# Kernel tuning notes

Hardware: AMD Instinct MI355X
Metric: run time of the kernel (lower is better)

Reference implementation:

```python
import jax, jax.numpy as jnp
import numpy as np

N = 100000   # nodes
E = 1600000  # edges
IN = 128     # input feature dim
HID = 64     # hidden = IN // 2
OUT = 8      # output_size
B = 16384    # lookup batch


def sage_conv(x, src, dst, W_l, W_r, b, n):
    # PyG SAGEConv (aggr='mean', root_weight=True):
    # out = lin_l(mean_{j in N(i)} x_j) + lin_r(x_i)
    msgs = x[src]                                              # [E, F] gather
    agg = jax.ops.segment_sum(msgs, dst, num_segments=n)       # [N, F] scatter-add
    deg = jax.ops.segment_sum(jnp.ones((src.shape[0],), x.dtype), dst, num_segments=n)
    mean = agg / jnp.maximum(deg, 1.0)[:, None]                # zero-degree -> 0
    return mean @ W_l + x @ W_r + b


def setup_inputs() -> dict:
    key = jax.random.key(0)
    ks = jax.random.split(key, 10)
    node_feats = jax.random.normal(ks[0], (N, IN), dtype=jnp.float32)
    edge_index = jax.random.randint(ks[1], (2, E), 0, N, dtype=jnp.int64)
    idx = jax.random.randint(ks[2], (B,), 0, N, dtype=jnp.int64)
    dropout_mask = jax.random.uniform(ks[3], (N, HID), dtype=jnp.float32)
    s1 = 1.0 / np.sqrt(IN)
    s2 = 1.0 / np.sqrt(HID)
    W1_l = jax.random.normal(ks[4], (IN, HID), dtype=jnp.float32) * s1
    W1_r = jax.random.normal(ks[5], (IN, HID), dtype=jnp.float32) * s1
    b1 = jnp.zeros((HID,), dtype=jnp.float32)
    W2_l = jax.random.normal(ks[6], (HID, OUT), dtype=jnp.float32) * s2
    W2_r = jax.random.normal(ks[7], (HID, OUT), dtype=jnp.float32) * s2
    b2 = jnp.zeros((OUT,), dtype=jnp.float32)
    return {"node_feats": node_feats, "edge_index": edge_index, "idx": idx,
            "dropout_mask": dropout_mask, "W1_l": W1_l, "W1_r": W1_r, "b1": b1,
            "W2_l": W2_l, "W2_r": W2_r, "b2": b2}


def reference(node_feats, edge_index, idx, dropout_mask, W1_l, W1_r, b1, W2_l, W2_r, b2):
    n = node_feats.shape[0]
    src, dst = edge_index[0], edge_index[1]
    h = sage_conv(node_feats, src, dst, W1_l, W1_r, b1, n)     # [N, HID]
    h = jax.nn.relu(h)
    keep = (dropout_mask > 0.5).astype(h.dtype)                # F.dropout p=0.5
    h = h * keep * 2.0                                         # inverted dropout scale 1/(1-p)
    emb = sage_conv(h, src, dst, W2_l, W2_r, b2, n)            # [N, OUT]
    return emb[idx]                                            # [B, OUT]
```

## Files before the change

kernel.cpp:

```cpp
#include <hip/hip_runtime.h>
#include <hip/hip_fp16.h>

#define IN_F 128
#define HID_F 64
#define OUT_F 8

#define BSHIFT 7
#define BGRAN 128
#define BCAP 2688
#define NBUK_MAX 784
#define CHUNK 4096
#define EPT (CHUNK / 256)
#define CEPT ((BCAP + 255) / 256)

#if defined(__has_builtin)
#if __has_builtin(__builtin_amdgcn_fdot2)
#define HAS_FDOT2 1
#endif
#endif

typedef _Float16 h2v __attribute__((ext_vector_type(2)));

__global__ __launch_bounds__(1024) void init_bcur(int* __restrict__ bcur, int nbuk) {
  int t = threadIdx.x;
  if (t < nbuk) bcur[t] = t * BCAP;
}

__global__ __launch_bounds__(256) void bucket_scatter(
    const int* __restrict__ src, const int* __restrict__ dst,
    int* __restrict__ bcur, int* __restrict__ ebuf, int n_edges) {
  __shared__ int hist[NBUK_MAX];
  __shared__ int base[NBUK_MAX];
  int t = threadIdx.x;
  for (int i = t; i < NBUK_MAX; i += 256) hist[i] = 0;
  __syncthreads();
  int e0 = blockIdx.x * CHUNK;
  int pk[EPT];
  int bk[EPT];
#pragma unroll
  for (int k = 0; k < EPT; ++k) {
    int e = e0 + k * 256 + t;
    if (e < n_edges) {
      int s = src[e];
      int d = dst[e];
      bk[k] = d >> BSHIFT;
      pk[k] = ((d & (BGRAN - 1)) << 24) | s;
      atomicAdd(&hist[bk[k]], 1);
    } else {
      bk[k] = -1;
    }
  }
  __syncthreads();
  for (int i = t; i < NBUK_MAX; i += 256) {
    int c = hist[i];
    base[i] = c ? atomicAdd(&bcur[i], c) : 0;
  }
  __syncthreads();
  for (int i = t; i < NBUK_MAX; i += 256) hist[i] = 0;
  __syncthreads();
#pragma unroll
  for (int k = 0; k < EPT; ++k) {
    if (bk[k] >= 0) {
      int r = atomicAdd(&hist[bk[k]], 1);
      ebuf[base[bk[k]] + r] = pk[k];
    }
  }
}

__global__ __launch_bounds__(256) void bucket_csr(
    const int* __restrict__ ebuf, const int* __restrict__ bcur,
    int* __restrict__ offs_f, int* __restrict__ deg_i,
    int* __restrict__ csr_src, int n_nodes) {
  __shared__ int hist[BGRAN];
  __shared__ int cur[BGRAN];
  __shared__ int s[BGRAN];
  __shared__ int lds_src[BCAP];
  int b = blockIdx.x;
  int t = threadIdx.x;
  if (t < BGRAN) hist[t] = 0;
  __syncthreads();
  int beg = b * BCAP;
  int cnt = bcur[b] - beg;
  int pk[CEPT];
  int np = 0;
  for (int j = t; j < cnt; j += 256) {
    pk[np] = ebuf[beg + j];
    atomicAdd(&hist[(unsigned)pk[np] >> 24], 1);
    ++np;
  }
  __syncthreads();
  if (t < BGRAN) s[t] = hist[t];
  __syncthreads();
  for (int d = 1; d < BGRAN; d <<= 1) {
    int v = 0;
    if (t >= d && t < BGRAN) v = s[t - d];
    __syncthreads();
    if (t >= d && t < BGRAN) s[t] += v;
    __syncthreads();
  }
  if (t < BGRAN) {
    int excl = (t == 0) ? 0 : s[t - 1];
    cur[t] = excl;
    int node = b * BGRAN + t;
    if (node < n_nodes) {
      offs_f[node] = beg + excl;
      deg_i[node] = hist[t];
    }
  }
  __syncthreads();
  for (int i = 0; i < np; ++i) {
    int dl = (unsigned)pk[i] >> 24;
    int p = atomicAdd(&cur[dl], 1);
    lds_src[p] = pk[i] & 0xFFFFFF;
  }
  __syncthreads();
  for (int j = t; j < cnt; j += 256) csr_src[beg + j] = lds_src[j];
}

#define BM 128
#define BK 32
__global__ __launch_bounds__(256, 4) void k1_proj(
    const float* __restrict__ x,
    const float* __restrict__ Wl,
    const float* __restrict__ Wr,
    const float* __restrict__ b1,
    const float* __restrict__ mask,
    __half* __restrict__ y1h,
    __half* __restrict__ r1h,
    unsigned long long* __restrict__ mbits,
    int n_nodes) {
  __shared__ h2v XS2[BK / 2][BM];
  __shared__ h2v WS2[BK / 2][128];
  int tid = threadIdx.x;
  int tx = tid & 15;
  int ty = tid >> 4;
  int n0 = blockIdx.x * BM;

  {
    int w = tid >> 6;
    int lane = tid & 63;
    for (int i = w; i < BM; i += 4) {
      int node = n0 + i;
      if (node < n_nodes) {
        float mv = mask[(size_t)node * HID_F + lane];
        unsigned long long bits = __ballot(mv > 0.5f);
        if (lane == 0) mbits[node] = bits;
      }
    }
  }

  float acc[8][8];
#pragma unroll
  for (int i = 0; i < 8; ++i)
#pragma unroll
    for (int j = 0; j < 8; ++j) acc[i][j] = 0.f;

  for (int kb = 0; kb < IN_F; kb += BK) {
    {
      int nn0 = tid >> 3;
      int k4 = (tid & 7) * 4;
      int kp0 = (tid & 7) * 2;
#pragma unroll
      for (int p = 0; p < 4; ++p) {
        int nn = nn0 + p * 32;
        int gs = min(n0 + nn, n_nodes - 1);
        float4 v = *(const float4*)(x + (size_t)gs * IN_F + kb + k4);
        XS2[kp0][nn] = h2v{(_Float16)v.x, (_Float16)v.y};
        XS2[kp0 + 1][nn] = h2v{(_Float16)v.z, (_Float16)v.w};
      }
    }
    {
#pragma unroll
      for (int p = 0; p < 2; ++p) {
        int sidx = tid + p * 256;
        int kp = sidx >> 5;
        int col = (sidx & 31) * 4;
        int k0 = kb + kp * 2;
        const float* pa = (col < 64) ? (Wl + (size_t)k0 * HID_F + col)
                                     : (Wr + (size_t)k0 * HID_F + (col - 64));
        const float* pb = (col < 64) ? (Wl + (size_t)(k0 + 1) * HID_F + col)
                                     : (Wr + (size_t)(k0 + 1) * HID_F + (col - 64));
        float4 wa = *(const float4*)pa;
        float4 wb = *(const float4*)pb;
        WS2[kp][col + 0] = h2v{(_Float16)wa.x, (_Float16)wb.x};
        WS2[kp][col + 1] = h2v{(_Float16)wa.y, (_Float16)wb.y};
        WS2[kp][col + 2] = h2v{(_Float16)wa.z, (_Float16)wb.z};
        WS2[kp][col + 3] = h2v{(_Float16)wa.w, (_Float16)wb.w};
      }
    }
    __syncthreads();
#pragma unroll 4
    for (int kp = 0; kp < BK / 2; ++kp) {
      h2v xv[8], wv[8];
#pragma unroll
      for (int i = 0; i < 8; ++i) xv[i] = XS2[kp][ty * 8 + i];
#pragma unroll
      for (int j = 0; j < 8; ++j) wv[j] = WS2[kp][tx * 8 + j];
#pragma unroll
      for (int i = 0; i < 8; ++i)
#pragma unroll
        for (int j = 0; j < 8; ++j) {
#ifdef HAS_FDOT2
          acc[i][j] = __builtin_amdgcn_fdot2(xv[i], wv[j], acc[i][j], false);
#else
          acc[i][j] += (float)xv[i][0] * (float)wv[j][0] +
                       (float)xv[i][1] * (float)wv[j][1];
#endif
        }
    }
    __syncthreads();
  }

  int outb = tx * 8;
  bool isR = (outb >= HID_F);
  int ob = isR ? outb - HID_F : outb;
  __half* dbuf = isR ? r1h : y1h;
  float bb[8];
#pragma unroll
  for (int j = 0; j < 8; ++j) bb[j] = isR ? b1[ob + j] : 0.f;
#pragma unroll
  for (int i = 0; i < 8; ++i) {
    int node = n0 + ty * 8 + i;
    if (node < n_nodes) {
      __half hh[8];
#pragma unroll
      for (int j = 0; j < 8; ++j) hh[j] = __float2half(acc[i][j] + bb[j]);
      *(uint4*)(dbuf + (size_t)node * HID_F + ob) = *(uint4*)hh;
    }
  }
}

__global__ __launch_bounds__(256) void agg1_fused(
    const __half* __restrict__ y1h,
    const __half* __restrict__ r1h,
    const int* __restrict__ deg_i,
    const int* __restrict__ offs,
    const int* __restrict__ csr_src,
    const unsigned long long* __restrict__ mbits,
    __half* __restrict__ h_h,
    int n_nodes) {
  int node = (blockIdx.x * blockDim.x + threadIdx.x) >> 6;
  int lane = threadIdx.x & 63;
  if (node >= n_nodes) return;
  int q = lane >> 4;
  int f4 = lane & 15;
  int beg = offs[node];
  int d = deg_i[node];
  const int* cp = csr_src + beg;
  float a0 = 0.f, a1 = 0.f, a2 = 0.f, a3 = 0.f;
  int j = 0;
  for (; j + 16 <= d; j += 16) {
    int s0 = cp[j + q];
    int s1 = cp[j + 4 + q];
    int s2 = cp[j + 8 + q];
    int s3 = cp[j + 12 + q];
    uint2 g0 = *(const uint2*)(y1h + (size_t)s0 * HID_F + f4 * 4);
    uint2 g1 = *(const uint2*)(y1h + (size_t)s1 * HID_F + f4 * 4);
    uint2 g2 = *(const uint2*)(y1h + (size_t)s2 * HID_F + f4 * 4);
    uint2 g3 = *(const uint2*)(y1h + (size_t)s3 * HID_F + f4 * 4);
    float2 p0 = __half22float2(*(const __half2*)&g0.x);
    float2 p1 = __half22float2(*(const __half2*)&g0.y);
    float2 p2 = __half22float2(*(const __half2*)&g1.x);
    float2 p3 = __half22float2(*(const __half2*)&g1.y);
    float2 p4 = __half22float2(*(const __half2*)&g2.x);
    float2 p5 = __half22float2(*(const __half2*)&g2.y);
    float2 p6 = __half22float2(*(const __half2*)&g3.x);
    float2 p7 = __half22float2(*(const __half2*)&g3.y);
    a0 += (p0.x + p2.x) + (p4.x + p6.x);
    a1 += (p0.y + p2.y) + (p4.y + p6.y);
    a2 += (p1.x + p3.x) + (p5.x + p7.x);
    a3 += (p1.y + p3.y) + (p5.y + p7.y);
  }
  for (; j < d; j += 4) {
    int e = j + q;
    if (e < d) {
      int s = cp[e];
      uint2 g = *(const uint2*)(y1h + (size_t)s * HID_F + f4 * 4);
      float2 p0 = __half22float2(*(const __half2*)&g.x);
      float2 p1 = __half22float2(*(const __half2*)&g.y);
      a0 += p0.x; a1 += p0.y; a2 += p1.x; a3 += p1.y;
    }
  }
  a0 += __shfl_xor(a0, 16); a0 += __shfl_xor(a0, 32);
  a1 += __shfl_xor(a1, 16); a1 += __shfl_xor(a1, 32);
  a2 += __shfl_xor(a2, 16); a2 += __shfl_xor(a2, 32);
  a3 += __shfl_xor(a3, 16); a3 += __shfl_xor(a3, 32);
  if (q == 0) {
    float inv = 1.0f / fmaxf((float)d, 1.0f);
    size_t o = (size_t)node * HID_F + f4 * 4;
    uint2 rg = *(const uint2*)(r1h + o);
    float2 r01 = __half22float2(*(const __half2*)&rg.x);
    float2 r23 = __half22float2(*(const __half2*)&rg.y);
    unsigned long long mb = mbits[node];
    float vx = fmaxf(a0 * inv + r01.x, 0.f);
    float vy = fmaxf(a1 * inv + r01.y, 0.f);
    float vz = fmaxf(a2 * inv + r23.x, 0.f);
    float vw = fmaxf(a3 * inv + r23.y, 0.f);
    int fb = f4 * 4;
    vx = ((mb >> (fb + 0)) & 1ull) ? vx * 2.f : 0.f;
    vy = ((mb >> (fb + 1)) & 1ull) ? vy * 2.f : 0.f;
    vz = ((mb >> (fb + 2)) & 1ull) ? vz * 2.f : 0.f;
    vw = ((mb >> (fb + 3)) & 1ull) ? vw * 2.f : 0.f;
    __half hh[4] = {__float2half(vx), __float2half(vy),
                    __float2half(vz), __float2half(vw)};
    *(uint2*)(h_h + o) = *(uint2*)hh;
  }
}

__global__ __launch_bounds__(256) void k3b_z(
    const __half* __restrict__ h_h,
    const float* __restrict__ W2l,
    __half* __restrict__ z,
    int n_nodes) {
  __shared__ float WS[HID_F][OUT_F];
  int tid = threadIdx.x;
  if (tid < 128) {
    float4 w = *(const float4*)(W2l + tid * 4);
    *(float4*)&WS[tid >> 1][(tid & 1) * 4] = w;
  }
  __syncthreads();
  int node = blockIdx.x * blockDim.x + tid;
  if (node >= n_nodes) return;
  const __half* hr = h_h + (size_t)node * HID_F;
  float acc[8] = {0, 0, 0, 0, 0, 0, 0, 0};
  for (int k = 0; k < HID_F; k += 8) {
    uint4 hv = *(const uint4*)(hr + k);
    float2 f0 = __half22float2(*(const __half2*)&hv.x);
    float2 f1 = __half22float2(*(const __half2*)&hv.y);
    float2 f2 = __half22float2(*(const __half2*)&hv.z);
    float2 f3 = __half22float2(*(const __half2*)&hv.w);
    float hh[8] = {f0.x, f0.y, f1.x, f1.y, f2.x, f2.y, f3.x, f3.y};
#pragma unroll
    for (int j = 0; j < 8; ++j) {
      float4 w0 = *(const float4*)&WS[k + j][0];
      float4 w1 = *(const float4*)&WS[k + j][4];
      acc[0] += hh[j] * w0.x; acc[1] += hh[j] * w0.y;
      acc[2] += hh[j] * w0.z; acc[3] += hh[j] * w0.w;
      acc[4] += hh[j] * w1.x; acc[5] += hh[j] * w1.y;
      acc[6] += hh[j] * w1.z; acc[7] += hh[j] * w1.w;
    }
  }
  __half hz[8];
#pragma unroll
  for (int j = 0; j < 8; ++j) hz[j] = __float2half(acc[j]);
  *(uint4*)(z + (size_t)node * OUT_F) = *(uint4*)hz;
}

__global__ __launch_bounds__(256) void out_fused(
    const int* __restrict__ idx,
    const __half* __restrict__ z,
    const int* __restrict__ deg_i,
    const int* __restrict__ offs,
    const int* __restrict__ csr_src,
    const __half* __restrict__ h_h,
    const float* __restrict__ W2r,
    const float* __restrict__ b2,
    float* __restrict__ out,
    int n_batch) {
  int b = (blockIdx.x * blockDim.x + threadIdx.x) >> 6;
  int lane = threadIdx.x & 63;
  if (b >= n_batch) return;
  int i = idx[b];
  int e8 = lane >> 3;
  int o = lane & 7;
  int beg = offs[i];
  int d = deg_i[i];
  float acc = 0.f;
  for (int j = e8; j < d; j += 8) {
    int s = csr_src[beg + j];
    acc += __half2float(z[(size_t)s * OUT_F + o]);
  }
  float dv = fmaxf((float)d, 1.0f);
  float v = acc / dv;
  uint4 hv = *(const uint4*)(h_h + (size_t)i * HID_F + e8 * 8);
  float2 f0 = __half22float2(*(const __half2*)&hv.x);
  float2 f1 = __half22float2(*(const __half2*)&hv.y);
  float2 f2 = __half22float2(*(const __half2*)&hv.z);
  float2 f3 = __half22float2(*(const __half2*)&hv.w);
  float hh[8] = {f0.x, f0.y, f1.x, f1.y, f2.x, f2.y, f3.x, f3.y};
#pragma unroll
  for (int jj = 0; jj < 8; ++jj) {
    int k = e8 * 8 + jj;
    v += hh[jj] * W2r[k * OUT_F + o];
  }
  v += __shfl_xor(v, 8);
  v += __shfl_xor(v, 16);
  v += __shfl_xor(v, 32);
  if (e8 == 0) out[(size_t)b * OUT_F + o] = v + b2[o];
}

extern "C" void kernel_launch(void* const* d_in, const int* in_sizes, int n_in,
                              void* d_out, int out_size, void* d_ws, size_t ws_size,
                              hipStream_t stream) {
  const float* x    = (const float*)d_in[0];
  const int*   ei   = (const int*)d_in[1];
  const int*   idx  = (const int*)d_in[2];
  const float* mask = (const float*)d_in[3];
  const float* W1l  = (const float*)d_in[4];
  const float* W1r  = (const float*)d_in[5];
  const float* b1   = (const float*)d_in[6];
  const float* W2l  = (const float*)d_in[7];
  const float* W2r  = (const float*)d_in[8];
  const float* b2   = (const float*)d_in[9];
  float* out = (float*)d_out;

  int n_nodes = in_sizes[0] / IN_F;
  int n_edges = in_sizes[1] / 2;
  int n_batch = in_sizes[2];
  const int* src = ei;
  const int* dst = ei + n_edges;

  int nbuk = (n_nodes + BGRAN - 1) / BGRAN;
  int nchunk = (n_edges + CHUNK - 1) / CHUNK;

  char* ws = (char*)d_ws;
  size_t off = 0;
  __half* y1h = (__half*)(ws + off); off += (size_t)n_nodes * HID_F * 2;
  __half* r1h = (__half*)(ws + off); off += (size_t)n_nodes * HID_F * 2;
  __half* h_h = (__half*)(ws + off); off += (size_t)n_nodes * HID_F * 2;
  __half* z   = (__half*)(ws + off); off += (size_t)n_nodes * OUT_F * 2;
  unsigned long long* mbits = (unsigned long long*)(ws + off); off += (size_t)n_nodes * 8;
  int* ebuf    = (int*)(ws + off); off += (size_t)nbuk * BCAP * 4;
  int* csr_src = (int*)(ws + off); off += (size_t)nbuk * BCAP * 4;
  int* deg_i   = (int*)(ws + off); off += (size_t)n_nodes * 4;
  int* offs_f  = (int*)(ws + off); off += (size_t)n_nodes * 4;
  int* bcur    = (int*)(ws + off); off += NBUK_MAX * 4;

  init_bcur<<<1, 1024, 0, stream>>>(bcur, nbuk);
  bucket_scatter<<<nchunk, 256, 0, stream>>>(src, dst, bcur, ebuf, n_edges);
  k1_proj<<<(n_nodes + BM - 1) / BM, 256, 0, stream>>>(
      x, W1l, W1r, b1, mask, y1h, r1h, mbits, n_nodes);
  bucket_csr<<<nbuk, 256, 0, stream>>>(ebuf, bcur, offs_f, deg_i, csr_src, n_nodes);

  {
    long long th = (long long)n_nodes * HID_F;
    agg1_fused<<<(int)((th + 255) / 256), 256, 0, stream>>>(
        y1h, r1h, deg_i, offs_f, csr_src, mbits, h_h, n_nodes);
  }

  k3b_z<<<(n_nodes + 255) / 256, 256, 0, stream>>>(h_h, W2l, z, n_nodes);
  {
    long long th = (long long)n_batch * 64;
    out_fused<<<(int)((th + 255) / 256), 256, 0, stream>>>(
        idx, z, deg_i, offs_f, csr_src, h_h, W2r, b2, out, n_batch);
  }
}
```

Measured before the change: 267.2 us.

## Use MFMA 16x16x32 f16 for layer-1 projection with pre-transposed fp16 weights

Replaces the fdot2-based register-tiled GEMM in k1_proj with MFMA 16x16x32 f16 instructions. Each wave computes 16 rows against all 128 output columns. A new w_prep kernel transposes and converts W1_l/W1_r to fp16 once per call, and B fragments are read directly from global memory. The x tile is staged in padded LDS in a single pass. This should cut ALU time for the projection, but output stores become scalar half writes and it adds a small serial prep kernel.

```diff
diff --git a/kernel.cpp b/kernel.cpp
--- a/kernel.cpp
+++ b/kernel.cpp
@@ -13,13 +13,8 @@
 #define EPT (CHUNK / 256)
 #define CEPT ((BCAP + 255) / 256)
 
-#if defined(__has_builtin)
-#if __has_builtin(__builtin_amdgcn_fdot2)
-#define HAS_FDOT2 1
-#endif
-#endif
-
-typedef _Float16 h2v __attribute__((ext_vector_type(2)));
+typedef _Float16 f16x8 __attribute__((ext_vector_type(8)));
+typedef float f32x4 __attribute__((ext_vector_type(4)));
 
 __global__ __launch_bounds__(1024) void init_bcur(int* __restrict__ bcur, int nbuk) {
   int t = threadIdx.x;
@@ -117,115 +112,86 @@
   for (int j = t; j < cnt; j += 256) csr_src[beg + j] = lds_src[j];
 }
 
-#define BM 128
-#define BK 32
-__global__ __launch_bounds__(256, 4) void k1_proj(
+__global__ __launch_bounds__(128) void w_prep(
+    const float* __restrict__ Wl, const float* __restrict__ Wr,
+    _Float16* __restrict__ Wt) {
+  int n = threadIdx.x;
+  for (int k = 0; k < IN_F; ++k) {
+    float v = (n < HID_F) ? Wl[k * HID_F + n] : Wr[k * HID_F + (n - HID_F)];
+    Wt[n * IN_F + k] = (_Float16)v;
+  }
+}
+
+#define K1_ROWS 64
+#define XSTRIDE 136
+__global__ __launch_bounds__(256) void k1_proj(
     const float* __restrict__ x,
-    const float* __restrict__ Wl,
-    const float* __restrict__ Wr,
+    const _Float16* __restrict__ Wt,
     const float* __restrict__ b1,
     const float* __restrict__ mask,
     __half* __restrict__ y1h,
     __half* __restrict__ r1h,
     unsigned long long* __restrict__ mbits,
     int n_nodes) {
-  __shared__ h2v XS2[BK / 2][BM];
-  __shared__ h2v WS2[BK / 2][128];
+  __shared__ _Float16 XS[K1_ROWS * XSTRIDE];
   int tid = threadIdx.x;
-  int tx = tid & 15;
-  int ty = tid >> 4;
-  int n0 = blockIdx.x * BM;
-
-  {
-    int w = tid >> 6;
-    int lane = tid & 63;
-    for (int i = w; i < BM; i += 4) {
-      int node = n0 + i;
-      if (node < n_nodes) {
-        float mv = mask[(size_t)node * HID_F + lane];
-        unsigned long long bits = __ballot(mv > 0.5f);
-        if (lane == 0) mbits[node] = bits;
-      }
-    }
-  }
-
-  float acc[8][8];
-#pragma unroll
-  for (int i = 0; i < 8; ++i)
-#pragma unroll
-    for (int j = 0; j < 8; ++j) acc[i][j] = 0.f;
-
-  for (int kb = 0; kb < IN_F; kb += BK) {
-    {
-      int nn0 = tid >> 3;
-      int k4 = (tid & 7) * 4;
-      int kp0 = (tid & 7) * 2;
-#pragma unroll
-      for (int p = 0; p < 4; ++p) {
-        int nn = nn0 + p * 32;
-        int gs = min(n0 + nn, n_nodes - 1);
-        float4 v = *(const float4*)(x + (size_t)gs * IN_F + kb + k4);
-        XS2[kp0][nn] = h2v{(_Float16)v.x, (_Float16)v.y};
-        XS2[kp0 + 1][nn] = h2v{(_Float16)v.z, (_Float16)v.w};
-      }
-    }
-    {
-#pragma unroll
-      for (int p = 0; p < 2; ++p) {
-        int sidx = tid + p * 256;
-        int kp = sidx >> 5;
-        int col = (sidx & 31) * 4;
-        int k0 = kb + kp * 2;
-        const float* pa = (col < 64) ? (Wl + (size_t)k0 * HID_F + col)
-                                     : (Wr + (size_t)k0 * HID_F + (col - 64));
-        const float* pb = (col < 64) ? (Wl + (size_t)(k0 + 1) * HID_F + col)
-                                     : (Wr + (size_t)(k0 + 1) * HID_F + (col - 64));
-        float4 wa = *(const float4*)pa;
-        float4 wb = *(const float4*)pb;
-        WS2[kp][col + 0] = h2v{(_Float16)wa.x, (_Float16)wb.x};
-        WS2[kp][col + 1] = h2v{(_Float16)wa.y, (_Float16)wb.y};
-        WS2[kp][col + 2] = h2v{(_Float16)wa.z, (_Float16)wb.z};
-        WS2[kp][col + 3] = h2v{(_Float16)wa.w, (_Float16)wb.w};
-      }
-    }
-    __syncthreads();
-#pragma unroll 4
-    for (int kp = 0; kp < BK / 2; ++kp) {
-      h2v xv[8], wv[8];
-#pragma unroll
-      for (int i = 0; i < 8; ++i) xv[i] = XS2[kp][ty * 8 + i];
-#pragma unroll
-      for (int j = 0; j < 8; ++j) wv[j] = WS2[kp][tx * 8 + j];
-#pragma unroll
-      for (int i = 0; i < 8; ++i)
-#pragma unroll
-        for (int j = 0; j < 8; ++j) {
-#ifdef HAS_FDOT2
-          acc[i][j] = __builtin_amdgcn_fdot2(xv[i], wv[j], acc[i][j], false);
-#else
-          acc[i][j] += (float)xv[i][0] * (float)wv[j][0] +
-                       (float)xv[i][1] * (float)wv[j][1];
-#endif
-        }
-    }
-    __syncthreads();
-  }
-
-  int outb = tx * 8;
-  bool isR = (outb >= HID_F);
-  int ob = isR ? outb - HID_F : outb;
-  __half* dbuf = isR ? r1h : y1h;
-  float bb[8];
-#pragma unroll
-  for (int j = 0; j < 8; ++j) bb[j] = isR ? b1[ob + j] : 0.f;
-#pragma unroll
-  for (int i = 0; i < 8; ++i) {
-    int node = n0 + ty * 8 + i;
+  int w = tid >> 6;
+  int lane = tid & 63;
+  int n0 = blockIdx.x * K1_ROWS;
+
+  for (int i = w * 16; i < w * 16 + 16; ++i) {
+    int node = n0 + i;
     if (node < n_nodes) {
-      __half hh[8];
-#pragma unroll
-      for (int j = 0; j < 8; ++j) hh[j] = __float2half(acc[i][j] + bb[j]);
-      *(uint4*)(dbuf + (size_t)node * HID_F + ob) = *(uint4*)hh;
+      float mv = mask[(size_t)node * HID_F + lane];
+      unsigned long long bits = __ballot(mv > 0.5f);
+      if (lane == 0) mbits[node] = bits;
+    }
+  }
+
+#pragma unroll
+  for (int p = 0; p < 8; ++p) {
+    int i = tid + p * 256;
+    int row = i >> 5;
+    int k4 = (i & 31) * 4;
+    int gs = min(n0 + row, n_nodes - 1);
+    float4 v = *(const float4*)(x + (size_t)gs * IN_F + k4);
+    _Float16 hv[4] = {(_Float16)v.x, (_Float16)v.y, (_Float16)v.z, (_Float16)v.w};
+    *(uint2*)&XS[row * XSTRIDE + k4] = *(uint2*)hv;
+  }
+  __syncthreads();
+
+  int m = lane & 15;
+  int quad = lane >> 4;
+
+  f32x4 acc[8];
+#pragma unroll
+  for (int t = 0; t < 8; ++t) acc[t] = f32x4{0.f, 0.f, 0.f, 0.f};
+
+#pragma unroll
+  for (int kk = 0; kk < 4; ++kk) {
+    f16x8 a = *(const f16x8*)&XS[(w * 16 + m) * XSTRIDE + kk * 32 + quad * 8];
+#pragma unroll
+    for (int t = 0; t < 8; ++t) {
+      f16x8 b = *(const f16x8*)(Wt + ((size_t)(t * 16 + m) * IN_F) + kk * 32 + quad * 8);
+      acc[t] = __builtin_amdgcn_mfma_f32_16x16x32_f16(a, b, acc[t], 0, 0, 0);
+    }
+  }
+
+  float bb[4];
+#pragma unroll
+  for (int t = 4; t < 8; ++t) bb[t - 4] = b1[(t - 4) * 16 + m];
+
+#pragma unroll
+  for (int t = 0; t < 8; ++t) {
+    bool isR = (t >= 4);
+    int col = isR ? (t - 4) * 16 + m : t * 16 + m;
+    __half* dbuf = isR ? r1h : y1h;
+    float badd = isR ? bb[t - 4] : 0.f;
+#pragma unroll
+    for (int r = 0; r < 4; ++r) {
+      int node = n0 + w * 16 + quad * 4 + r;
+      if (node < n_nodes)
+        dbuf[(size_t)node * HID_F + col] = __float2half(acc[t][r] + badd);
     }
   }
 }
@@ -420,6 +386,7 @@
   __half* h_h = (__half*)(ws + off); off += (size_t)n_nodes * HID_F * 2;
   __half* z   = (__half*)(ws + off); off += (size_t)n_nodes * OUT_F * 2;
   unsigned long long* mbits = (unsigned long long*)(ws + off); off += (size_t)n_nodes * 8;
+  _Float16* Wt = (_Float16*)(ws + off); off += (size_t)IN_F * IN_F * 2;
   int* ebuf    = (int*)(ws + off); off += (size_t)nbuk * BCAP * 4;
   int* csr_src = (int*)(ws + off); off += (size_t)nbuk * BCAP * 4;
   int* deg_i   = (int*)(ws + off); off += (size_t)n_nodes * 4;
@@ -427,9 +394,10 @@
   int* bcur    = (int*)(ws + off); off += NBUK_MAX * 4;
 
   init_bcur<<<1, 1024, 0, stream>>>(bcur, nbuk);
+  w_prep<<<1, 128, 0, stream>>>(W1l, W1r, Wt);
   bucket_scatter<<<nchunk, 256, 0, stream>>>(src, dst, bcur, ebuf, n_edges);
-  k1_proj<<<(n_nodes + BM - 1) / BM, 256, 0, stream>>>(
-      x, W1l, W1r, b1, mask, y1h, r1h, mbits, n_nodes);
+  k1_proj<<<(n_nodes + K1_ROWS - 1) / K1_ROWS, 256, 0, stream>>>(
+      x, Wt, b1, mask, y1h, r1h, mbits, n_nodes);
   bucket_csr<<<nbuk, 256, 0, stream>>>(ebuf, bcur, offs_f, deg_i, csr_src, n_nodes);
 
   {
```

Result: slower. 280.6 us (+5.0%).
